# Optimization experiments

Measured on AMD Instinct MI355X. Metric: run time of the kernel, lower is better.

The kernel has to match this reference:

```python
import jax, jax.numpy as jnp
import numpy as np

HEAD_DIM = 128
NUM_Q_HEADS = 32
NUM_KV_HEADS = 8
HIDDEN = HEAD_DIM * NUM_Q_HEADS  # 4096
ROPE_BASE = 10000.0


def setup_inputs() -> dict:
    key = jax.random.key(0)
    k1, k2, k3, k4, k5 = jax.random.split(key, 5)
    B, S = 1, 2048
    scale = 0.02  # keep activations sane given integer-valued x
    input_ids = jax.random.randint(k5, (B, S), 0, 100, dtype=jnp.int64) if jax.config.jax_enable_x64 else jax.random.randint(k5, (B, S), 0, 100, dtype=jnp.int32)
    position_ids = (jnp.arange(B * S).reshape(B, S) % S).astype(input_ids.dtype)
    Wq = jax.random.normal(k1, (HIDDEN, NUM_Q_HEADS * HEAD_DIM), dtype=jnp.float32) * scale
    Wk = jax.random.normal(k2, (HIDDEN, NUM_KV_HEADS * HEAD_DIM), dtype=jnp.float32) * scale
    Wv = jax.random.normal(k3, (HIDDEN, NUM_KV_HEADS * HEAD_DIM), dtype=jnp.float32) * scale
    Wo = jax.random.normal(k4, (NUM_Q_HEADS * HEAD_DIM, HIDDEN), dtype=jnp.float32) * scale
    return {"input_ids": input_ids, "position_ids": position_ids,
            "Wq": Wq, "Wk": Wk, "Wv": Wv, "Wo": Wo}


def _rotate_half(x):
    x1, x2 = jnp.split(x, 2, axis=-1)
    return jnp.concatenate([-x2, x1], axis=-1)


def _cos_sin(position_ids):
    # standard RoPE cos/sin, shape [B, S, 1, head_dim]
    inv_freq = 1.0 / (ROPE_BASE ** (jnp.arange(0, HEAD_DIM, 2, dtype=jnp.float32) / HEAD_DIM))
    ang = position_ids.astype(jnp.float32)[..., None] * inv_freq  # [B,S,d/2]
    cos = jnp.concatenate([jnp.cos(ang), jnp.cos(ang)], axis=-1)[:, :, None, :]
    sin = jnp.concatenate([jnp.sin(ang), jnp.sin(ang)], axis=-1)[:, :, None, :]
    return cos, sin


def reference(input_ids, position_ids, Wq, Wk, Wv, Wo):
    B, S = input_ids.shape
    # x = input_ids broadcast to hidden_size (as in the torch model)
    x = jnp.broadcast_to(input_ids[..., None].astype(jnp.float32), (B, S, HIDDEN))
    q = (x @ Wq).reshape(B, S, NUM_Q_HEADS, HEAD_DIM)
    k = (x @ Wk).reshape(B, S, NUM_KV_HEADS, HEAD_DIM)
    v = (x @ Wv).reshape(B, S, NUM_KV_HEADS, HEAD_DIM)
    cos, sin = _cos_sin(position_ids)
    q = q * cos + _rotate_half(q) * sin
    k = k * cos + _rotate_half(k) * sin
    # GQA: group q heads over kv heads
    G = NUM_Q_HEADS // NUM_KV_HEADS
    qg = q.reshape(B, S, NUM_KV_HEADS, G, HEAD_DIM)
    scores = jnp.einsum('bqhgd,bkhd->bhgqk', qg, k) / jnp.sqrt(jnp.float32(HEAD_DIM))
    causal = jnp.tril(jnp.ones((S, S), dtype=bool))  # [S_q, S_k]
    scores = jnp.where(causal, scores, -jnp.inf)
    attn = jax.nn.softmax(scores, axis=-1)
    out = jnp.einsum('bhgqk,bkhd->bqhgd', attn, v).reshape(B, S, NUM_Q_HEADS * HEAD_DIM)
    return out @ Wo
```

## Files before the change

### kernel.cpp

```cpp
#include <hip/hip_runtime.h>
#include <math.h>


#define HID 4096
#define NQH 32
#define NKVH 8
#define HD 128
#define CH 64
#define RSQRT_HD 0.08838834764831845f
#define SQRT_HD  11.313708498984761f

__device__ __forceinline__ void colsum_part(const float* __restrict__ W,
                                            float* __restrict__ P,
                                            int cols4, int c4, int chunk) {
    const float4* b = reinterpret_cast<const float4*>(W);
    float ax = 0.f, ay = 0.f, az = 0.f, aw = 0.f;
#pragma unroll
    for (int bb = 0; bb < 8; ++bb) {
        size_t p = (size_t)(chunk * 64 + bb * 8) * cols4 + c4;
        float4 t0 = b[p];
        float4 t1 = b[p + 1 * (size_t)cols4];
        float4 t2 = b[p + 2 * (size_t)cols4];
        float4 t3 = b[p + 3 * (size_t)cols4];
        float4 t4 = b[p + 4 * (size_t)cols4];
        float4 t5 = b[p + 5 * (size_t)cols4];
        float4 t6 = b[p + 6 * (size_t)cols4];
        float4 t7 = b[p + 7 * (size_t)cols4];
        ax += ((t0.x + t1.x) + (t2.x + t3.x)) + ((t4.x + t5.x) + (t6.x + t7.x));
        ay += ((t0.y + t1.y) + (t2.y + t3.y)) + ((t4.y + t5.y) + (t6.y + t7.y));
        az += ((t0.z + t1.z) + (t2.z + t3.z)) + ((t4.z + t5.z) + (t6.z + t7.z));
        aw += ((t0.w + t1.w) + (t2.w + t3.w)) + ((t4.w + t5.w) + (t6.w + t7.w));
    }
    reinterpret_cast<float4*>(P)[(size_t)chunk * cols4 + c4] =
        make_float4(ax, ay, az, aw);
}

__global__ __launch_bounds__(256) void k_part(
        const int* __restrict__ ids,
        const float* __restrict__ Wq, const float* __restrict__ Wk,
        const float* __restrict__ Wv,
        float* __restrict__ Pq, float* __restrict__ Pk, float* __restrict__ Pv,
        float* __restrict__ cp, double* __restrict__ Tc, double* __restrict__ Ts,
        int S) {
    int t = blockIdx.x;
    int tid = threadIdx.x;
    int nxb = S >> 8;
    int trigT = 64 * nxb;
    if (t < trigT) {
        int j = t / nxb, xb = t - j * nxb;
        int dlt = xb * 256 + tid;
        double f = (double)(float)(1.0 / pow(10000.0, (double)j / 64.0));
        double sv, cv;
        sincos((double)dlt * f, &sv, &cv);
        Tc[(size_t)j * S + dlt] = cv;
        Ts[(size_t)j * S + dlt] = sv;
        if (j == 0) cp[dlt] = (float)ids[dlt] * RSQRT_HD;
    } else if (t < trigT + 4 * CH) {
        int u = t - trigT;
        colsum_part(Wq, Pq, NQH * HD / 4, (u & 3) * 256 + tid, u >> 2);
    } else if (t < trigT + 5 * CH) {
        colsum_part(Wk, Pk, NKVH * HD / 4, tid, t - trigT - 4 * CH);
    } else {
        colsum_part(Wv, Pv, NKVH * HD / 4, tid, t - trigT - 5 * CH);
    }
}

__global__ __launch_bounds__(256) void k_red(
        const float* __restrict__ Pq, const float* __restrict__ Pk,
        const float* __restrict__ Pv, float* __restrict__ Sq,
        float* __restrict__ Sk, float* __restrict__ Sv) {
    int t = blockIdx.x;
    const float* P; float* Sd; int cols4, c4;
    if (t < 4)      { P = Pq; Sd = Sq; cols4 = NQH * HD / 4; c4 = t * 256 + threadIdx.x; }
    else if (t == 4){ P = Pk; Sd = Sk; cols4 = NKVH * HD / 4; c4 = threadIdx.x; }
    else            { P = Pv; Sd = Sv; cols4 = NKVH * HD / 4; c4 = threadIdx.x; }
    const float4* b = reinterpret_cast<const float4*>(P);
    float4 a = make_float4(0.f, 0.f, 0.f, 0.f);
#pragma unroll 8
    for (int c = 0; c < CH; ++c) {
        float4 v = b[(size_t)c * cols4 + c4];
        a.x += v.x; a.y += v.y; a.z += v.z; a.w += v.w;
    }
    reinterpret_cast<float4*>(Sd)[c4] = a;
}

__global__ __launch_bounds__(256) void k_main(
        const float* __restrict__ Sq, const float* __restrict__ Sk,
        const float* __restrict__ Sv, const float* __restrict__ Wo,
        const double* __restrict__ Tc, const double* __restrict__ Ts,
        float* __restrict__ M, float* __restrict__ D, int S) {
    int t = blockIdx.x;
    int tid = threadIdx.x;
    if (t < 128) {
        int hg = t >> 2, x = t & 3, h = hg >> 2;
        int i4 = x * 256 + tid;
        const float4* b = reinterpret_cast<const float4*>(Wo);
        float ax = 0.f, ay = 0.f, az = 0.f, aw = 0.f;
        for (int d0 = 0; d0 < HD; d0 += 8) {
            size_t p = (size_t)(hg * HD + d0) * (HID / 4) + i4;
            float s0 = Sv[h * HD + d0 + 0], s1 = Sv[h * HD + d0 + 1];
            float s2 = Sv[h * HD + d0 + 2], s3 = Sv[h * HD + d0 + 3];
            float s4 = Sv[h * HD + d0 + 4], s5 = Sv[h * HD + d0 + 5];
            float s6 = Sv[h * HD + d0 + 6], s7 = Sv[h * HD + d0 + 7];
            float4 t0 = b[p];
            float4 t1 = b[p + 1 * (size_t)(HID / 4)];
            float4 t2 = b[p + 2 * (size_t)(HID / 4)];
            float4 t3 = b[p + 3 * (size_t)(HID / 4)];
            float4 t4 = b[p + 4 * (size_t)(HID / 4)];
            float4 t5 = b[p + 5 * (size_t)(HID / 4)];
            float4 t6 = b[p + 6 * (size_t)(HID / 4)];
            float4 t7 = b[p + 7 * (size_t)(HID / 4)];
            ax += ((s0 * t0.x + s1 * t1.x) + (s2 * t2.x + s3 * t3.x)) +
                  ((s4 * t4.x + s5 * t5.x) + (s6 * t6.x + s7 * t7.x));
            ay += ((s0 * t0.y + s1 * t1.y) + (s2 * t2.y + s3 * t3.y)) +
                  ((s4 * t4.y + s5 * t5.y) + (s6 * t6.y + s7 * t7.y));
            az += ((s0 * t0.z + s1 * t1.z) + (s2 * t2.z + s3 * t3.z)) +
                  ((s4 * t4.z + s5 * t5.z) + (s6 * t6.z + s7 * t7.z));
            aw += ((s0 * t0.w + s1 * t1.w) + (s2 * t2.w + s3 * t3.w)) +
                  ((s4 * t4.w + s5 * t5.w) + (s6 * t6.w + s7 * t7.w));
        }
        reinterpret_cast<float4*>(M)[(size_t)hg * (HID / 4) + i4] =
            make_float4(ax, ay, az, aw);
    } else {
        __shared__ double p[64], q[64];
        int u = t - 128;
        int nxb = S >> 8;
        int hg = u / nxb, xb = u - hg * nxb, h = hg >> 2;
        if (tid < 64) {
            double a1 = Sq[hg * HD + tid], a2 = Sq[hg * HD + tid + 64];
            double b1 = Sk[h * HD + tid],  b2 = Sk[h * HD + tid + 64];
            p[tid] = a1 * b1 + a2 * b2;
            q[tid] = a2 * b1 - a1 * b2;
        }
        __syncthreads();
        int dlt = xb * 256 + tid;
        const double* tc = Tc + dlt;
        const double* ts = Ts + dlt;
        double acc = 0.0;
#pragma unroll 8
        for (int j = 0; j < 64; ++j)
            acc += p[j] * tc[(size_t)j * S] - q[j] * ts[(size_t)j * S];
        D[(size_t)hg * S + dlt] = (float)acc;
    }
}

__global__ __launch_bounds__(256) void k_alpha(
        const int* __restrict__ ids, const float* __restrict__ cp,
        const float* __restrict__ D, float* __restrict__ A, int S) {
    int w = blockIdx.x * 4 + (threadIdx.x >> 6);
    int lane = threadIdx.x & 63;
    int s = S - 1 - (w >> 5);
    int hg = w & 31;
    float cs = (float)ids[s];
    const float* Drow = D + (size_t)hg * S;
    const float* cps = cp + s;

    float m = -INFINITY, se = 0.f, sp = 0.f;
    int n = s + 1;
    int nFull = n >> 8;
    for (int it = 0; it < nFull; ++it) {
        int d0 = it * 256 + lane * 4;
        float4 dv = *reinterpret_cast<const float4*>(Drow + d0);
        float c0 = cps[-(d0 + 0)], c1 = cps[-(d0 + 1)];
        float c2 = cps[-(d0 + 2)], c3 = cps[-(d0 + 3)];
        float z0 = cs * (c0 * dv.x), z1 = cs * (c1 * dv.y);
        float z2 = cs * (c2 * dv.z), z3 = cs * (c3 * dv.w);
        float zc = fmaxf(fmaxf(z0, z1), fmaxf(z2, z3));
        if (!__all(zc <= m)) {
            float r = __expf(fminf(m - zc, 0.f));
            se *= r; sp *= r; m = fmaxf(m, zc);
        }
        float e0 = __expf(z0 - m), e1 = __expf(z1 - m);
        float e2 = __expf(z2 - m), e3 = __expf(z3 - m);
        se += (e0 + e1) + (e2 + e3);
        sp += e0 * c0 + e1 * c1 + e2 * c2 + e3 * c3;
    }
    if (n & 255) {
        int d0 = nFull * 256 + lane * 4;
        float4 dv = *reinterpret_cast<const float4*>(Drow + d0);
        float c0 = cps[-(d0 + 0)], c1 = cps[-(d0 + 1)];
        float c2 = cps[-(d0 + 2)], c3 = cps[-(d0 + 3)];
        float z0 = (d0 + 0 < n) ? cs * (c0 * dv.x) : -INFINITY;
        float z1 = (d0 + 1 < n) ? cs * (c1 * dv.y) : -INFINITY;
        float z2 = (d0 + 2 < n) ? cs * (c2 * dv.z) : -INFINITY;
        float z3 = (d0 + 3 < n) ? cs * (c3 * dv.w) : -INFINITY;
        float zc = fmaxf(fmaxf(z0, z1), fmaxf(z2, z3));
        float r = __expf(fminf(m - zc, 0.f));
        se *= r; sp *= r; m = fmaxf(m, zc);
        float mm = fmaxf(m, -1e30f);
        float e0 = __expf(z0 - mm), e1 = __expf(z1 - mm);
        float e2 = __expf(z2 - mm), e3 = __expf(z3 - mm);
        se += (e0 + e1) + (e2 + e3);
        sp += e0 * c0 + e1 * c1 + e2 * c2 + e3 * c3;
    }
    for (int o = 32; o; o >>= 1) {
        float mo = __shfl_xor(m, o);
        float so = __shfl_xor(se, o);
        float po = __shfl_xor(sp, o);
        float M = fmaxf(m, mo);
        float e1 = __expf(fminf(m - M, 0.f));
        float e2 = __expf(fminf(mo - M, 0.f));
        se = se * e1 + so * e2;
        sp = sp * e1 + po * e2;
        m = M;
    }
    if (lane == 0) A[(size_t)s * NQH + hg] = SQRT_HD * sp / se;
}

__global__ void k_out(const float* __restrict__ A, const float* __restrict__ M,
                      float* __restrict__ out, int S) {
    __shared__ float a[512];
    int tid = threadIdx.x;
    int s0 = blockIdx.y * 16;
    a[tid] = A[(size_t)s0 * NQH + tid];
    a[tid + 256] = A[(size_t)s0 * NQH + tid + 256];
    __syncthreads();
    int i = blockIdx.x * 256 + tid;
    float acc[16];
#pragma unroll
    for (int r = 0; r < 16; ++r) acc[r] = 0.f;
    for (int hg = 0; hg < NQH; ++hg) {
        float mv = M[(size_t)hg * HID + i];
#pragma unroll
        for (int r = 0; r < 16; ++r) acc[r] += a[r * NQH + hg] * mv;
    }
#pragma unroll
    for (int r = 0; r < 16; ++r)
        out[(size_t)(s0 + r) * HID + i] = acc[r];
}

extern "C" void kernel_launch(void* const* d_in, const int* in_sizes, int n_in,
                              void* d_out, int out_size, void* d_ws, size_t ws_size,
                              hipStream_t stream) {
    const int*   ids = (const int*)d_in[0];
    const float* Wq  = (const float*)d_in[2];
    const float* Wk  = (const float*)d_in[3];
    const float* Wv  = (const float*)d_in[4];
    const float* Wo  = (const float*)d_in[5];
    float* out = (float*)d_out;
    const int S = in_sizes[0];

    float* ws = (float*)d_ws;
    float* Pq = ws;
    float* Pk = Pq + (size_t)CH * NQH * HD;
    float* Pv = Pk + (size_t)CH * NKVH * HD;
    float* M  = ws;
    float* Sq = Pv + (size_t)CH * NKVH * HD;
    float* Sk = Sq + HID;
    float* Sv = Sk + NKVH * HD;
    float* D  = Sv + NKVH * HD;
    float* cp = D + (size_t)NQH * S;
    float* A  = cp + S;
    double* Tc = (double*)(A + (size_t)NQH * S);
    double* Ts = Tc + (size_t)64 * S;

    int nxb = S >> 8;
    k_part<<<64 * nxb + 6 * CH, 256, 0, stream>>>(
        ids, Wq, Wk, Wv, Pq, Pk, Pv, cp, Tc, Ts, S);
    k_red<<<6, 256, 0, stream>>>(Pq, Pk, Pv, Sq, Sk, Sv);
    k_main<<<128 + NQH * nxb, 256, 0, stream>>>(Sq, Sk, Sv, Wo, Tc, Ts, M, D, S);
    k_alpha<<<S * 8, 256, 0, stream>>>(ids, cp, D, A, S);
    k_out<<<dim3(HID / 256, S / 16), 256, 0, stream>>>(A, M, out, S);
}
```

Measured before the change: 104.5 us.

## Split weight reductions finer, fuse Wo matvec with softmax kernel, use shifted cp copies

Doubles the number of column-sum chunks for Wq/Wk/Wv so more blocks stream the weights in parallel. The Wo·Sv matvec is split four ways over the head dimension, with partials summed in k_out, and moved into the same launch as the softmax/alpha kernel so it overlaps with that work. Four shifted, zero-padded copies of the scaled ids are built so the reversed cp accesses become aligned float4 loads. The softmax loop is unrolled by two and uses exp2 with log2e prescaling. This adds extra partial buffers, an extra reduction in k_out, and a larger setup kernel.

New measurement: 94.81 us. 1.1x faster.

```diff
diff --git a/kernel.cpp b/kernel.cpp
--- a/kernel.cpp
+++ b/kernel.cpp
@@ -6,30 +6,30 @@
 #define NQH 32
 #define NKVH 8
 #define HD 128
-#define CH 64
+#define CHQ 128
 #define RSQRT_HD 0.08838834764831845f
 #define SQRT_HD  11.313708498984761f
-
-__device__ __forceinline__ void colsum_part(const float* __restrict__ W,
-                                            float* __restrict__ P,
-                                            int cols4, int c4, int chunk) {
+#define LOG2E    1.4426950408889634f
+
+__device__ __forceinline__ void colsum_part32(const float* __restrict__ W,
+                                              float* __restrict__ P,
+                                              int cols4, int c4, int chunk) {
     const float4* b = reinterpret_cast<const float4*>(W);
     float ax = 0.f, ay = 0.f, az = 0.f, aw = 0.f;
 #pragma unroll
-    for (int bb = 0; bb < 8; ++bb) {
-        size_t p = (size_t)(chunk * 64 + bb * 8) * cols4 + c4;
-        float4 t0 = b[p];
-        float4 t1 = b[p + 1 * (size_t)cols4];
-        float4 t2 = b[p + 2 * (size_t)cols4];
-        float4 t3 = b[p + 3 * (size_t)cols4];
-        float4 t4 = b[p + 4 * (size_t)cols4];
-        float4 t5 = b[p + 5 * (size_t)cols4];
-        float4 t6 = b[p + 6 * (size_t)cols4];
-        float4 t7 = b[p + 7 * (size_t)cols4];
-        ax += ((t0.x + t1.x) + (t2.x + t3.x)) + ((t4.x + t5.x) + (t6.x + t7.x));
-        ay += ((t0.y + t1.y) + (t2.y + t3.y)) + ((t4.y + t5.y) + (t6.y + t7.y));
-        az += ((t0.z + t1.z) + (t2.z + t3.z)) + ((t4.z + t5.z) + (t6.z + t7.z));
-        aw += ((t0.w + t1.w) + (t2.w + t3.w)) + ((t4.w + t5.w) + (t6.w + t7.w));
+    for (int bb = 0; bb < 4; ++bb) {
+        size_t p = (size_t)(chunk * 32 + bb * 8) * cols4 + c4;
+        float4 tt[8];
+#pragma unroll
+        for (int i = 0; i < 8; ++i) tt[i] = b[p + (size_t)i * cols4];
+        ax += ((tt[0].x + tt[1].x) + (tt[2].x + tt[3].x)) +
+              ((tt[4].x + tt[5].x) + (tt[6].x + tt[7].x));
+        ay += ((tt[0].y + tt[1].y) + (tt[2].y + tt[3].y)) +
+              ((tt[4].y + tt[5].y) + (tt[6].y + tt[7].y));
+        az += ((tt[0].z + tt[1].z) + (tt[2].z + tt[3].z)) +
+              ((tt[4].z + tt[5].z) + (tt[6].z + tt[7].z));
+        aw += ((tt[0].w + tt[1].w) + (tt[2].w + tt[3].w)) +
+              ((tt[4].w + tt[5].w) + (tt[6].w + tt[7].w));
     }
     reinterpret_cast<float4*>(P)[(size_t)chunk * cols4 + c4] =
         make_float4(ax, ay, az, aw);
@@ -40,28 +40,35 @@
         const float* __restrict__ Wq, const float* __restrict__ Wk,
         const float* __restrict__ Wv,
         float* __restrict__ Pq, float* __restrict__ Pk, float* __restrict__ Pv,
-        float* __restrict__ cp, double* __restrict__ Tc, double* __restrict__ Ts,
-        int S) {
+        float* __restrict__ cpsh, double* __restrict__ Tc,
+        double* __restrict__ Ts, int S) {
     int t = blockIdx.x;
     int tid = threadIdx.x;
     int nxb = S >> 8;
-    int trigT = 64 * nxb;
-    if (t < trigT) {
-        int j = t / nxb, xb = t - j * nxb;
+    if (t < 4 * CHQ) {
+        colsum_part32(Wq, Pq, NQH * HD / 4, (t & 3) * 256 + tid, t >> 2);
+    } else if (t < 5 * CHQ) {
+        colsum_part32(Wk, Pk, NKVH * HD / 4, tid, t - 4 * CHQ);
+    } else if (t < 6 * CHQ) {
+        colsum_part32(Wv, Pv, NKVH * HD / 4, tid, t - 5 * CHQ);
+    } else if (t < 6 * CHQ + 64 * nxb) {
+        int u = t - 6 * CHQ;
+        int j = u / nxb, xb = u - j * nxb;
         int dlt = xb * 256 + tid;
         double f = (double)(float)(1.0 / pow(10000.0, (double)j / 64.0));
         double sv, cv;
         sincos((double)dlt * f, &sv, &cv);
         Tc[(size_t)j * S + dlt] = cv;
         Ts[(size_t)j * S + dlt] = sv;
-        if (j == 0) cp[dlt] = (float)ids[dlt] * RSQRT_HD;
-    } else if (t < trigT + 4 * CH) {
-        int u = t - trigT;
-        colsum_part(Wq, Pq, NQH * HD / 4, (u & 3) * 256 + tid, u >> 2);
-    } else if (t < trigT + 5 * CH) {
-        colsum_part(Wk, Pk, NKVH * HD / 4, tid, t - trigT - 4 * CH);
     } else {
-        colsum_part(Wv, Pv, NKVH * HD / 4, tid, t - trigT - 5 * CH);
+        int u = t - 6 * CHQ - 64 * nxb;
+        int r = u >> 2, seg = u & 3;
+        int LEN = S + 768;
+        for (int pos = seg * 256 + tid; pos < LEN; pos += 1024) {
+            int i = pos - 384 - r;
+            float v = (i >= 0 && i < S) ? (float)ids[i] * RSQRT_HD : 0.f;
+            cpsh[(size_t)r * LEN + pos] = v;
+        }
     }
 }
 
@@ -75,139 +82,163 @@
     else if (t == 4){ P = Pk; Sd = Sk; cols4 = NKVH * HD / 4; c4 = threadIdx.x; }
     else            { P = Pv; Sd = Sv; cols4 = NKVH * HD / 4; c4 = threadIdx.x; }
     const float4* b = reinterpret_cast<const float4*>(P);
-    float4 a = make_float4(0.f, 0.f, 0.f, 0.f);
+    float ax = 0.f, ay = 0.f, az = 0.f, aw = 0.f;
+    for (int c = 0; c < CHQ; c += 8) {
+        float4 tt[8];
+#pragma unroll
+        for (int i = 0; i < 8; ++i) tt[i] = b[(size_t)(c + i) * cols4 + c4];
+        ax += ((tt[0].x + tt[1].x) + (tt[2].x + tt[3].x)) +
+              ((tt[4].x + tt[5].x) + (tt[6].x + tt[7].x));
+        ay += ((tt[0].y + tt[1].y) + (tt[2].y + tt[3].y)) +
+              ((tt[4].y + tt[5].y) + (tt[6].y + tt[7].y));
+        az += ((tt[0].z + tt[1].z) + (tt[2].z + tt[3].z)) +
+              ((tt[4].z + tt[5].z) + (tt[6].z + tt[7].z));
+        aw += ((tt[0].w + tt[1].w) + (tt[2].w + tt[3].w)) +
+              ((tt[4].w + tt[5].w) + (tt[6].w + tt[7].w));
+    }
+    reinterpret_cast<float4*>(Sd)[c4] = make_float4(ax, ay, az, aw);
+}
+
+__global__ __launch_bounds__(256) void k_dtab(
+        const float* __restrict__ Sq, const float* __restrict__ Sk,
+        const double* __restrict__ Tc, const double* __restrict__ Ts,
+        float* __restrict__ D, int S) {
+    __shared__ double p[64], q[64];
+    int hg = blockIdx.y, h = hg >> 2;
+    int tid = threadIdx.x;
+    if (tid < 64) {
+        double a1 = Sq[hg * HD + tid], a2 = Sq[hg * HD + tid + 64];
+        double b1 = Sk[h * HD + tid],  b2 = Sk[h * HD + tid + 64];
+        p[tid] = a1 * b1 + a2 * b2;
+        q[tid] = a2 * b1 - a1 * b2;
+    }
+    __syncthreads();
+    int dlt = blockIdx.x * 256 + tid;
+    const double* tc = Tc + dlt;
+    const double* ts = Ts + dlt;
+    double acc = 0.0;
 #pragma unroll 8
-    for (int c = 0; c < CH; ++c) {
-        float4 v = b[(size_t)c * cols4 + c4];
-        a.x += v.x; a.y += v.y; a.z += v.z; a.w += v.w;
-    }
-    reinterpret_cast<float4*>(Sd)[c4] = a;
-}
-
-__global__ __launch_bounds__(256) void k_main(
-        const float* __restrict__ Sq, const float* __restrict__ Sk,
-        const float* __restrict__ Sv, const float* __restrict__ Wo,
-        const double* __restrict__ Tc, const double* __restrict__ Ts,
-        float* __restrict__ M, float* __restrict__ D, int S) {
+    for (int j = 0; j < 64; ++j)
+        acc += p[j] * tc[(size_t)j * S] - q[j] * ts[(size_t)j * S];
+    D[(size_t)hg * S + dlt] = (float)acc;
+}
+
+__global__ __launch_bounds__(256) void k_fuse(
+        const int* __restrict__ ids, const float* __restrict__ cpsh,
+        const float* __restrict__ D, const float* __restrict__ Sv,
+        const float* __restrict__ Wo, float* __restrict__ Mp,
+        float* __restrict__ A, int S) {
     int t = blockIdx.x;
     int tid = threadIdx.x;
-    if (t < 128) {
-        int hg = t >> 2, x = t & 3, h = hg >> 2;
+    if (t < 512) {
+        int sl = t & 3, x = (t >> 2) & 3, hg = t >> 4;
+        int h = hg >> 2, dbase = hg * HD + sl * 32;
         int i4 = x * 256 + tid;
         const float4* b = reinterpret_cast<const float4*>(Wo);
+        const float* sv = Sv + h * HD + sl * 32;
         float ax = 0.f, ay = 0.f, az = 0.f, aw = 0.f;
-        for (int d0 = 0; d0 < HD; d0 += 8) {
-            size_t p = (size_t)(hg * HD + d0) * (HID / 4) + i4;
-            float s0 = Sv[h * HD + d0 + 0], s1 = Sv[h * HD + d0 + 1];
-            float s2 = Sv[h * HD + d0 + 2], s3 = Sv[h * HD + d0 + 3];
-            float s4 = Sv[h * HD + d0 + 4], s5 = Sv[h * HD + d0 + 5];
-            float s6 = Sv[h * HD + d0 + 6], s7 = Sv[h * HD + d0 + 7];
-            float4 t0 = b[p];
-            float4 t1 = b[p + 1 * (size_t)(HID / 4)];
-            float4 t2 = b[p + 2 * (size_t)(HID / 4)];
-            float4 t3 = b[p + 3 * (size_t)(HID / 4)];
-            float4 t4 = b[p + 4 * (size_t)(HID / 4)];
-            float4 t5 = b[p + 5 * (size_t)(HID / 4)];
-            float4 t6 = b[p + 6 * (size_t)(HID / 4)];
-            float4 t7 = b[p + 7 * (size_t)(HID / 4)];
-            ax += ((s0 * t0.x + s1 * t1.x) + (s2 * t2.x + s3 * t3.x)) +
-                  ((s4 * t4.x + s5 * t5.x) + (s6 * t6.x + s7 * t7.x));
-            ay += ((s0 * t0.y + s1 * t1.y) + (s2 * t2.y + s3 * t3.y)) +
-                  ((s4 * t4.y + s5 * t5.y) + (s6 * t6.y + s7 * t7.y));
-            az += ((s0 * t0.z + s1 * t1.z) + (s2 * t2.z + s3 * t3.z)) +
-                  ((s4 * t4.z + s5 * t5.z) + (s6 * t6.z + s7 * t7.z));
-            aw += ((s0 * t0.w + s1 * t1.w) + (s2 * t2.w + s3 * t3.w)) +
-                  ((s4 * t4.w + s5 * t5.w) + (s6 * t6.w + s7 * t7.w));
-        }
-        reinterpret_cast<float4*>(M)[(size_t)hg * (HID / 4) + i4] =
+#pragma unroll
+        for (int bb = 0; bb < 4; ++bb) {
+            size_t p = (size_t)(dbase + bb * 8) * (HID / 4) + i4;
+            float4 tt[8]; float ss[8];
+#pragma unroll
+            for (int i = 0; i < 8; ++i) { tt[i] = b[p + (size_t)i * (HID / 4)]; ss[i] = sv[bb * 8 + i]; }
+#pragma unroll
+            for (int i = 0; i < 8; ++i) {
+                ax += ss[i] * tt[i].x; ay += ss[i] * tt[i].y;
+                az += ss[i] * tt[i].z; aw += ss[i] * tt[i].w;
+            }
+        }
+        reinterpret_cast<float4*>(Mp)[((size_t)sl * NQH + hg) * (HID / 4) + i4] =
             make_float4(ax, ay, az, aw);
-    } else {
-        __shared__ double p[64], q[64];
-        int u = t - 128;
-        int nxb = S >> 8;
-        int hg = u / nxb, xb = u - hg * nxb, h = hg >> 2;
-        if (tid < 64) {
-            double a1 = Sq[hg * HD + tid], a2 = Sq[hg * HD + tid + 64];
-            double b1 = Sk[h * HD + tid],  b2 = Sk[h * HD + tid + 64];
-            p[tid] = a1 * b1 + a2 * b2;
-            q[tid] = a2 * b1 - a1 * b2;
-        }
-        __syncthreads();
-        int dlt = xb * 256 + tid;
-        const double* tc = Tc + dlt;
-        const double* ts = Ts + dlt;
-        double acc = 0.0;
-#pragma unroll 8
-        for (int j = 0; j < 64; ++j)
-            acc += p[j] * tc[(size_t)j * S] - q[j] * ts[(size_t)j * S];
-        D[(size_t)hg * S + dlt] = (float)acc;
-    }
-}
-
-__global__ __launch_bounds__(256) void k_alpha(
-        const int* __restrict__ ids, const float* __restrict__ cp,
-        const float* __restrict__ D, float* __restrict__ A, int S) {
-    int w = blockIdx.x * 4 + (threadIdx.x >> 6);
-    int lane = threadIdx.x & 63;
+        return;
+    }
+    int u = t - 512;
+    int w = u * 4 + (tid >> 6);
+    int lane = tid & 63;
     int s = S - 1 - (w >> 5);
     int hg = w & 31;
-    float cs = (float)ids[s];
+    float csl = (float)ids[s] * LOG2E;
     const float* Drow = D + (size_t)hg * S;
-    const float* cps = cp + s;
+    int r = (3 - s) & 3;
+    const float* cbase = cpsh + (size_t)r * (S + 768) + 384 + (s - 3 + r);
 
     float m = -INFINITY, se = 0.f, sp = 0.f;
     int n = s + 1;
     int nFull = n >> 8;
-    for (int it = 0; it < nFull; ++it) {
+    int it = 0;
+    for (; it + 2 <= nFull; it += 2) {
+        int d0 = it * 256 + lane * 4, d1 = d0 + 256;
+        float4 dv0 = *reinterpret_cast<const float4*>(Drow + d0);
+        float4 dv1 = *reinterpret_cast<const float4*>(Drow + d1);
+        float4 cv0 = *reinterpret_cast<const float4*>(cbase - d0);
+        float4 cv1 = *reinterpret_cast<const float4*>(cbase - d1);
+        float z0 = csl * (cv0.w * dv0.x), z1 = csl * (cv0.z * dv0.y);
+        float z2 = csl * (cv0.y * dv0.z), z3 = csl * (cv0.x * dv0.w);
+        float z4 = csl * (cv1.w * dv1.x), z5 = csl * (cv1.z * dv1.y);
+        float z6 = csl * (cv1.y * dv1.z), z7 = csl * (cv1.x * dv1.w);
+        float zc = fmaxf(fmaxf(fmaxf(z0, z1), fmaxf(z2, z3)),
+                         fmaxf(fmaxf(z4, z5), fmaxf(z6, z7)));
+        if (!__all(zc <= m)) {
+            float rr = __builtin_amdgcn_exp2f(fminf(m - zc, 0.f));
+            se *= rr; sp *= rr; m = fmaxf(m, zc);
+        }
+        float e0 = __builtin_amdgcn_exp2f(z0 - m), e1 = __builtin_amdgcn_exp2f(z1 - m);
+        float e2 = __builtin_amdgcn_exp2f(z2 - m), e3 = __builtin_amdgcn_exp2f(z3 - m);
+        float e4 = __builtin_amdgcn_exp2f(z4 - m), e5 = __builtin_amdgcn_exp2f(z5 - m);
+        float e6 = __builtin_amdgcn_exp2f(z6 - m), e7 = __builtin_amdgcn_exp2f(z7 - m);
+        se += ((e0 + e1) + (e2 + e3)) + ((e4 + e5) + (e6 + e7));
+        sp += ((e0 * cv0.w + e1 * cv0.z) + (e2 * cv0.y + e3 * cv0.x)) +
+              ((e4 * cv1.w + e5 * cv1.z) + (e6 * cv1.y + e7 * cv1.x));
+    }
+    if (it < nFull) {
         int d0 = it * 256 + lane * 4;
-        float4 dv = *reinterpret_cast<const float4*>(Drow + d0);
-        float c0 = cps[-(d0 + 0)], c1 = cps[-(d0 + 1)];
-        float c2 = cps[-(d0 + 2)], c3 = cps[-(d0 + 3)];
-        float z0 = cs * (c0 * dv.x), z1 = cs * (c1 * dv.y);
-        float z2 = cs * (c2 * dv.z), z3 = cs * (c3 * dv.w);
+        float4 dv0 = *reinterpret_cast<const float4*>(Drow + d0);
+        float4 cv0 = *reinterpret_cast<const float4*>(cbase - d0);
+        float z0 = csl * (cv0.w * dv0.x), z1 = csl * (cv0.z * dv0.y);
+        float z2 = csl * (cv0.y * dv0.z), z3 = csl * (cv0.x * dv0.w);
         float zc = fmaxf(fmaxf(z0, z1), fmaxf(z2, z3));
         if (!__all(zc <= m)) {
-            float r = __expf(fminf(m - zc, 0.f));
-            se *= r; sp *= r; m = fmaxf(m, zc);
-        }
-        float e0 = __expf(z0 - m), e1 = __expf(z1 - m);
-        float e2 = __expf(z2 - m), e3 = __expf(z3 - m);
+            float rr = __builtin_amdgcn_exp2f(fminf(m - zc, 0.f));
+            se *= rr; sp *= rr; m = fmaxf(m, zc);
+        }
+        float e0 = __builtin_amdgcn_exp2f(z0 - m), e1 = __builtin_amdgcn_exp2f(z1 - m);
+        float e2 = __builtin_amdgcn_exp2f(z2 - m), e3 = __builtin_amdgcn_exp2f(z3 - m);
         se += (e0 + e1) + (e2 + e3);
-        sp += e0 * c0 + e1 * c1 + e2 * c2 + e3 * c3;
+        sp += (e0 * cv0.w + e1 * cv0.z) + (e2 * cv0.y + e3 * cv0.x);
     }
     if (n & 255) {
         int d0 = nFull * 256 + lane * 4;
-        float4 dv = *reinterpret_cast<const float4*>(Drow + d0);
-        float c0 = cps[-(d0 + 0)], c1 = cps[-(d0 + 1)];
-        float c2 = cps[-(d0 + 2)], c3 = cps[-(d0 + 3)];
-        float z0 = (d0 + 0 < n) ? cs * (c0 * dv.x) : -INFINITY;
-        float z1 = (d0 + 1 < n) ? cs * (c1 * dv.y) : -INFINITY;
-        float z2 = (d0 + 2 < n) ? cs * (c2 * dv.z) : -INFINITY;
-        float z3 = (d0 + 3 < n) ? cs * (c3 * dv.w) : -INFINITY;
+        float4 dv0 = *reinterpret_cast<const float4*>(Drow + d0);
+        float4 cv0 = *reinterpret_cast<const float4*>(cbase - d0);
+        float z0 = (d0 + 0 < n) ? csl * (cv0.w * dv0.x) : -INFINITY;
+        float z1 = (d0 + 1 < n) ? csl * (cv0.z * dv0.y) : -INFINITY;
+        float z2 = (d0 + 2 < n) ? csl * (cv0.y * dv0.z) : -INFINITY;
+        float z3 = (d0 + 3 < n) ? csl * (cv0.x * dv0.w) : -INFINITY;
         float zc = fmaxf(fmaxf(z0, z1), fmaxf(z2, z3));
-        float r = __expf(fminf(m - zc, 0.f));
-        se *= r; sp *= r; m = fmaxf(m, zc);
+        float rr = __builtin_amdgcn_exp2f(fminf(m - zc, 0.f));
+        se *= rr; sp *= rr; m = fmaxf(m, zc);
         float mm = fmaxf(m, -1e30f);
-        float e0 = __expf(z0 - mm), e1 = __expf(z1 - mm);
-        float e2 = __expf(z2 - mm), e3 = __expf(z3 - mm);
+        float e0 = __builtin_amdgcn_exp2f(z0 - mm), e1 = __builtin_amdgcn_exp2f(z1 - mm);
+        float e2 = __builtin_amdgcn_exp2f(z2 - mm), e3 = __builtin_amdgcn_exp2f(z3 - mm);
         se += (e0 + e1) + (e2 + e3);
-        sp += e0 * c0 + e1 * c1 + e2 * c2 + e3 * c3;
+        sp += (e0 * cv0.w + e1 * cv0.z) + (e2 * cv0.y + e3 * cv0.x);
     }
     for (int o = 32; o; o >>= 1) {
         float mo = __shfl_xor(m, o);
         float so = __shfl_xor(se, o);
         float po = __shfl_xor(sp, o);
-        float M = fmaxf(m, mo);
-        float e1 = __expf(fminf(m - M, 0.f));
-        float e2 = __expf(fminf(mo - M, 0.f));
-        se = se * e1 + so * e2;
-        sp = sp * e1 + po * e2;
-        m = M;
+        float M2 = fmaxf(m, mo);
+        float ea = __builtin_amdgcn_exp2f(fminf(m - M2, 0.f));
+        float eb = __builtin_amdgcn_exp2f(fminf(mo - M2, 0.f));
+        se = se * ea + so * eb;
+        sp = sp * ea + po * eb;
+        m = M2;
     }
     if (lane == 0) A[(size_t)s * NQH + hg] = SQRT_HD * sp / se;
 }
 
-__global__ void k_out(const float* __restrict__ A, const float* __restrict__ M,
+__global__ void k_out(const float* __restrict__ A, const float* __restrict__ Mp,
                       float* __restrict__ out, int S) {
     __shared__ float a[512];
     int tid = threadIdx.x;
@@ -218,15 +249,18 @@
     int i = blockIdx.x * 256 + tid;
     float acc[16];
 #pragma unroll
-    for (int r = 0; r < 16; ++r) acc[r] = 0.f;
+    for (int rr = 0; rr < 16; ++rr) acc[rr] = 0.f;
     for (int hg = 0; hg < NQH; ++hg) {
-        float mv = M[(size_t)hg * HID + i];
-#pragma unroll
-        for (int r = 0; r < 16; ++r) acc[r] += a[r * NQH + hg] * mv;
-    }
-#pragma unroll
-    for (int r = 0; r < 16; ++r)
-        out[(size_t)(s0 + r) * HID + i] = acc[r];
+        float mv = Mp[(size_t)(0 * NQH + hg) * HID + i]
+                 + Mp[(size_t)(1 * NQH + hg) * HID + i]
+                 + Mp[(size_t)(2 * NQH + hg) * HID + i]
+                 + Mp[(size_t)(3 * NQH + hg) * HID + i];
+#pragma unroll
+        for (int rr = 0; rr < 16; ++rr) acc[rr] += a[rr * NQH + hg] * mv;
+    }
+#pragma unroll
+    for (int rr = 0; rr < 16; ++rr)
+        out[(size_t)(s0 + rr) * HID + i] = acc[rr];
 }
 
 extern "C" void kernel_launch(void* const* d_in, const int* in_sizes, int n_in,
@@ -239,26 +273,27 @@
     const float* Wo  = (const float*)d_in[5];
     float* out = (float*)d_out;
     const int S = in_sizes[0];
+    const int nxb = S >> 8;
+    const int LEN = S + 768;
 
     float* ws = (float*)d_ws;
     float* Pq = ws;
-    float* Pk = Pq + (size_t)CH * NQH * HD;
-    float* Pv = Pk + (size_t)CH * NKVH * HD;
-    float* M  = ws;
-    float* Sq = Pv + (size_t)CH * NKVH * HD;
+    float* Pk = Pq + (size_t)CHQ * NQH * HD;
+    float* Pv = Pk + (size_t)CHQ * NKVH * HD;
+    float* Mp = Pq;
+    float* Sq = Pv + (size_t)CHQ * NKVH * HD;
     float* Sk = Sq + HID;
     float* Sv = Sk + NKVH * HD;
     float* D  = Sv + NKVH * HD;
-    float* cp = D + (size_t)NQH * S;
-    float* A  = cp + S;
-    double* Tc = (double*)(A + (size_t)NQH * S);
+    float* A  = D + (size_t)NQH * S;
+    float* cpsh = A + (size_t)NQH * S;
+    double* Tc = (double*)(cpsh + 4 * (size_t)LEN);
     double* Ts = Tc + (size_t)64 * S;
 
-    int nxb = S >> 8;
-    k_part<<<64 * nxb + 6 * CH, 256, 0, stream>>>(
-        ids, Wq, Wk, Wv, Pq, Pk, Pv, cp, Tc, Ts, S);
+    k_part<<<6 * CHQ + 64 * nxb + 16, 256, 0, stream>>>(
+        ids, Wq, Wk, Wv, Pq, Pk, Pv, cpsh, Tc, Ts, S);
     k_red<<<6, 256, 0, stream>>>(Pq, Pk, Pv, Sq, Sk, Sv);
-    k_main<<<128 + NQH * nxb, 256, 0, stream>>>(Sq, Sk, Sv, Wo, Tc, Ts, M, D, S);
-    k_alpha<<<S * 8, 256, 0, stream>>>(ids, cp, D, A, S);
-    k_out<<<dim3(HID / 256, S / 16), 256, 0, stream>>>(A, M, out, S);
-}
+    k_dtab<<<dim3(nxb, NQH), 256, 0, stream>>>(Sq, Sk, Tc, Ts, D, S);
+    k_fuse<<<512 + S * 8, 256, 0, stream>>>(ids, cpsh, D, Sv, Wo, Mp, A, S);
+    k_out<<<dim3(HID / 256, S / 16), 256, 0, stream>>>(A, Mp, out, S);
+}
```
